# Kernel optimization log

Hardware: AMD Instinct MI355X
Metric: run time of the kernel (lower is better)

Reference implementation:

```python
import jax, jax.numpy as jnp
import numpy as np
import math

B, A, IN_C, OUT_C = 64, 128, 128, 64

def _l2norm(x, eps=1e-12):
    # matches F.normalize(dim=1) on 2D input: x / max(||x||_2, eps) along last dim
    n = jnp.sqrt(jnp.sum(x * x, axis=-1, keepdims=True))
    return x / jnp.maximum(n, eps)

def setup_inputs() -> dict:
    key = jax.random.key(0)
    ks = jax.random.split(key, 7)
    s = 1.0 / math.sqrt(IN_C)
    return {
        "features": jax.random.normal(ks[0], (B, IN_C, A), dtype=jnp.float32),
        "Wq": jax.random.uniform(ks[1], (OUT_C, IN_C), jnp.float32, -s, s),
        "bq": jax.random.uniform(ks[2], (OUT_C,), jnp.float32, -s, s),
        "Wk": jax.random.uniform(ks[3], (OUT_C, IN_C), jnp.float32, -s, s),
        "bk": jax.random.uniform(ks[4], (OUT_C,), jnp.float32, -s, s),
        "Wv": jax.random.uniform(ks[5], (OUT_C, IN_C), jnp.float32, -s, s),
        "bv": jax.random.uniform(ks[6], (OUT_C,), jnp.float32, -s, s),
    }

def reference(features, Wq, bq, Wk, bk, Wv, bv):
    b = features.shape[0]
    f = jnp.transpose(features, (0, 2, 1))          # (b, a, in_c)
    a = f.shape[1]
    q = f @ Wq.T + bq                               # (b, a, d)
    k = f @ Wk.T + bk
    v = f @ Wv.T + bv
    d = q.shape[-1]
    qf = q.reshape(-1, d)                           # (N, d), N = b*a
    kf = k.reshape(-1, d)
    vf = v.reshape(-1, d)
    att = jax.nn.softmax(qf @ kf.T / math.sqrt(d), axis=1)  # (N, N)
    qkv = att @ vf                                  # (N, d)
    qkv_n = _l2norm(qkv).reshape(b, a, d)
    v_n = _l2norm(vf).reshape(b, a, d)
    # sim_s[i,j] = (1/a) * sum_t v_n[i,t] . qkv_n[j,t]  (diagonal-trace over 'a')
    sim_s = jnp.einsum('bad,cad->bc', v_n, qkv_n) / a
    return sim_s
```

## Files before the change

### kernel.cpp

```cpp
#include <hip/hip_runtime.h>
#include <hip/hip_bf16.h>

#define NROW 8192
#define INC  128
#define OUTC 64

#define QSCALE 0.18033688011112042f

typedef __bf16 bf16x8 __attribute__((ext_vector_type(8)));
typedef __bf16 bf16x4 __attribute__((ext_vector_type(4)));
typedef short  s16x4  __attribute__((ext_vector_type(4)));
typedef float  f32x4  __attribute__((ext_vector_type(4)));

static __device__ __forceinline__ f32x4 mfma16(bf16x8 a, bf16x8 b, f32x4 c) {
    return __builtin_amdgcn_mfma_f32_16x16x32_bf16(a, b, c, 0, 0, 0);
}
static __device__ __forceinline__ f32x4 mfma1k(s16x4 a, s16x4 b, f32x4 c) {
    return __builtin_amdgcn_mfma_f32_16x16x16bf16_1k(a, b, c, 0, 0, 0);
}

static __device__ __forceinline__ bf16x8 cvt8(float4 lo, float4 hi) {
    bf16x8 r;
    r[0] = (__bf16)lo.x; r[1] = (__bf16)lo.y; r[2] = (__bf16)lo.z; r[3] = (__bf16)lo.w;
    r[4] = (__bf16)hi.x; r[5] = (__bf16)hi.y; r[6] = (__bf16)hi.z; r[7] = (__bf16)hi.w;
    return r;
}

__global__ __launch_bounds__(256) void proj_kernel(
    const float* __restrict__ feat,
    const float* __restrict__ Wq, const float* __restrict__ bq,
    const float* __restrict__ Wk, const float* __restrict__ bk,
    const float* __restrict__ Wv, const float* __restrict__ bv,
    __hip_bfloat16* __restrict__ qbf, __hip_bfloat16* __restrict__ kbf,
    __hip_bfloat16* __restrict__ vbf, __hip_bfloat16* __restrict__ vnb)
{
    __shared__ float slab[32 * 132];
    __shared__ float vbuf[32 * 66];
    __shared__ float invb[32];

    const int blk = blockIdx.x;
    const int mat = blk >> 8;
    const int b   = (blk >> 2) & 63;
    const int a0  = (blk & 3) * 32;
    const int r0  = b * 128 + a0;
    const float* fb = feat + (size_t)b * INC * 128;

    for (int i = threadIdx.x; i < 32 * 128; i += 256) {
        int c = i >> 5, a = i & 31;
        slab[a * 132 + c] = fb[c * 128 + a0 + a];
    }
    __syncthreads();

    const int w    = threadIdx.x >> 6;
    const int lane = threadIdx.x & 63;
    const int l16  = lane & 15;
    const int quad = lane >> 4;
    const int n0   = w * 16;

    const float* W    = (mat == 0) ? Wq : (mat == 1) ? Wk : Wv;
    const float* bias = (mat == 0) ? bq : (mat == 1) ? bk : bv;

    f32x4 acc[2] = {{0.f,0.f,0.f,0.f},{0.f,0.f,0.f,0.f}};
    #pragma unroll
    for (int kc = 0; kc < 4; ++kc) {
        const int k0 = kc * 32 + quad * 8;
        const float* wr = W + (n0 + l16) * INC + k0;
        bf16x8 bfr = cvt8(*(const float4*)wr, *(const float4*)(wr + 4));
        #pragma unroll
        for (int u = 0; u < 2; ++u) {
            const float* ar = slab + (u * 16 + l16) * 132 + k0;
            bf16x8 afr = cvt8(*(const float4*)ar, *(const float4*)(ar + 4));
            acc[u] = mfma16(afr, bfr, acc[u]);
        }
    }
    const float bl = bias[n0 + l16];
    const float sc = (mat == 0) ? QSCALE : 1.0f;

    if (mat < 2) {
        __hip_bfloat16* dst = mat ? kbf : qbf;
        #pragma unroll
        for (int u = 0; u < 2; ++u) {
            const int base = ((((r0 >> 4) + u) * 4 + w) << 8) + l16;
            #pragma unroll
            for (int r = 0; r < 4; ++r)
                dst[base + (quad * 4 + r) * 16] = __float2bfloat16((acc[u][r] + bl) * sc);
        }
    } else {
        #pragma unroll
        for (int u = 0; u < 2; ++u)
            #pragma unroll
            for (int r = 0; r < 4; ++r)
                vbuf[(u * 16 + quad * 4 + r) * 66 + n0 + l16] = acc[u][r] + bl;
        __syncthreads();
        const int rl = threadIdx.x >> 3;
        const int jj = threadIdx.x & 7;
        float ss = 0.f;
        #pragma unroll
        for (int i = 0; i < 8; ++i) {
            float x = vbuf[rl * 66 + jj * 8 + i];
            ss += x * x;
        }
        ss += __shfl_xor(ss, 1, 64);
        ss += __shfl_xor(ss, 2, 64);
        ss += __shfl_xor(ss, 4, 64);
        if (jj == 0) invb[rl] = rsqrtf(fmaxf(ss, 1e-24f));
        __syncthreads();
        float inv = invb[rl];
        bf16x8 vp;
        #pragma unroll
        for (int i = 0; i < 8; ++i)
            vp[i] = (__bf16)(vbuf[rl * 66 + jj * 8 + i] * inv);
        *(bf16x8*)(vnb + (size_t)(r0 + rl) * 64 + jj * 8) = vp;
        const int tl = threadIdx.x & 15;
        const int n  = (threadIdx.x >> 4) & 3;
        const int s_ = threadIdx.x >> 6;
        bf16x8 pack;
        #pragma unroll
        for (int j = 0; j < 8; ++j) {
            int key = s_ * 8 + j;
            pack[j] = (__bf16)(vbuf[key * 66 + n * 16 + tl] * invb[key]);
        }
        const int base = ((((r0 >> 4) + (s_ >> 1)) * 4 + n) << 8) + tl * 16 + (s_ & 1) * 8;
        *(bf16x8*)(vbf + base) = pack;
    }
}

__global__ __launch_bounds__(256) void attn_kernel(
    const __hip_bfloat16* __restrict__ qbf,
    const __hip_bfloat16* __restrict__ kbf,
    const __hip_bfloat16* __restrict__ vbf,
    float* __restrict__ Opart, float* __restrict__ lpart)
{
    const int qb    = blockIdx.x >> 3;
    const int bg    = blockIdx.x & 7;
    const int w     = threadIdx.x >> 6;
    const int lane  = threadIdx.x & 63;
    const int l16   = lane & 15;
    const int quad  = lane >> 4;
    const int r0    = qb * 128 + w * 32;
    const int fo    = l16 * 16 + quad * 4;
    const int fo32  = l16 * 16 + (quad & 1) * 8;
    const int qh    = quad >> 1;

    bf16x8 qf32[2][2];
    #pragma unroll
    for (int u = 0; u < 2; ++u)
        #pragma unroll
        for (int p = 0; p < 2; ++p)
            qf32[u][p] = *(const bf16x8*)(qbf +
                ((((r0 >> 4) + u) * 4 + p * 2 + qh) << 8) + fo32);

    f32x4 of[2][4];
    float lp[2] = {0.f, 0.f};
    #pragma unroll
    for (int u = 0; u < 2; ++u)
        #pragma unroll
        for (int n = 0; n < 4; ++n)
            of[u][n] = (f32x4){0.f, 0.f, 0.f, 0.f};

    const int ck0 = bg * 64;
    const char* kpA = (const char*)kbf + ck0 * 2048 + qh * 512 + fo32 * 2;
    const char* kpB = kpA + 4096;
    const char* vpA = (const char*)vbf + ck0 * 2048 + fo * 2;
    const char* vpB = vpA + 4096;

    #pragma unroll 1
    for (int it = 0; it < 16; ++it) {
        bf16x8 kf[4][2];
        #pragma unroll
        for (int t = 0; t < 2; ++t)
            #pragma unroll
            for (int p = 0; p < 2; ++p) {
                kf[t][p]     = *(const bf16x8*)(kpA + t * 2048 + p * 1024);
                kf[t + 2][p] = *(const bf16x8*)(kpB + t * 2048 + p * 1024);
            }
        s16x4 vf[4][4];
        #pragma unroll
        for (int n = 0; n < 4; ++n)
            #pragma unroll
            for (int t = 0; t < 2; ++t) {
                vf[n][t]     = *(const s16x4*)(vpA + t * 2048 + n * 512);
                vf[n][t + 2] = *(const s16x4*)(vpB + t * 2048 + n * 512);
            }
        kpA += 8192; kpB += 8192; vpA += 8192; vpB += 8192;

        const f32x4 zero = (f32x4){0.f, 0.f, 0.f, 0.f};
        #pragma unroll
        for (int u = 0; u < 2; ++u) {
            f32x4 s[4];
            #pragma unroll
            for (int t = 0; t < 4; ++t) {
                s[t] = mfma16(kf[t][0], qf32[u][0], zero);
                s[t] = mfma16(kf[t][1], qf32[u][1], s[t]);
            }
            #pragma unroll
            for (int t = 0; t < 4; ++t) {
                union { bf16x4 v; s16x4 s4; } pf;
                #pragma unroll
                for (int r = 0; r < 4; ++r) {
                    float p = __builtin_amdgcn_exp2f(s[t][r]);
                    lp[u] += p;
                    pf.v[r] = (__bf16)p;
                }
                #pragma unroll
                for (int n = 0; n < 4; ++n)
                    of[u][n] = mfma1k(pf.s4, vf[n][t], of[u][n]);
            }
        }
    }

    #pragma unroll
    for (int u = 0; u < 2; ++u) {
        float v = lp[u];
        v += __shfl_xor(v, 16, 64);
        v += __shfl_xor(v, 32, 64);
        lp[u] = v;
    }

    const int task = (qb * 4 + w) * 8 + bg;
    float* Ob = Opart + (size_t)task * 2048;
    #pragma unroll
    for (int u = 0; u < 2; ++u)
        #pragma unroll
        for (int n = 0; n < 4; ++n)
            #pragma unroll
            for (int r = 0; r < 4; ++r)
                Ob[(u * 16 + quad * 4 + r) * 64 + n * 16 + l16] = of[u][n][r];
    if (quad == 0) {
        lpart[task * 32 + l16]      = lp[0];
        lpart[task * 32 + 16 + l16] = lp[1];
    }
}

__global__ __launch_bounds__(256) void combine_kernel(
    const float* __restrict__ Opart, const float* __restrict__ lpart,
    __hip_bfloat16* __restrict__ qnb)
{
    const int r    = blockIdx.x * 4 + (threadIdx.x >> 6);
    const int c    = threadIdx.x & 63;
    const int tile = r >> 5, row = r & 31;
    float acc = 0.f, lsum = 0.f;
    #pragma unroll
    for (int g = 0; g < 8; ++g) {
        int task = tile * 8 + g;
        acc  += Opart[(size_t)task * 2048 + row * 64 + c];
        lsum += lpart[task * 32 + row];
    }
    float q = acc / lsum;
    float ss = q * q;
    ss += __shfl_xor(ss, 1, 64);
    ss += __shfl_xor(ss, 2, 64);
    ss += __shfl_xor(ss, 4, 64);
    ss += __shfl_xor(ss, 8, 64);
    ss += __shfl_xor(ss, 16, 64);
    ss += __shfl_xor(ss, 32, 64);
    qnb[(size_t)r * 64 + c] = __float2bfloat16(q * rsqrtf(fmaxf(ss, 1e-24f)));
}

__global__ __launch_bounds__(64) void sim_kernel(
    const __hip_bfloat16* __restrict__ vnb,
    const __hip_bfloat16* __restrict__ qnb,
    float* __restrict__ out)
{
    const int lane = threadIdx.x;
    const int l16  = lane & 15;
    const int quad = lane >> 4;
    const int kblk = blockIdx.x * 256;

    f32x4 acc[4][4];
    #pragma unroll
    for (int mi = 0; mi < 4; ++mi)
        #pragma unroll
        for (int ni = 0; ni < 4; ++ni)
            acc[mi][ni] = (f32x4){0.f, 0.f, 0.f, 0.f};

    #pragma unroll
    for (int ks = 0; ks < 8; ++ks) {
        const int k0 = kblk + ks * 32 + quad * 8;
        bf16x8 af[4], bfv[4];
        #pragma unroll
        for (int mi = 0; mi < 4; ++mi)
            af[mi] = *(const bf16x8*)(vnb + (size_t)(mi * 16 + l16) * 8192 + k0);
        #pragma unroll
        for (int ni = 0; ni < 4; ++ni)
            bfv[ni] = *(const bf16x8*)(qnb + (size_t)(ni * 16 + l16) * 8192 + k0);
        #pragma unroll
        for (int mi = 0; mi < 4; ++mi)
            #pragma unroll
            for (int ni = 0; ni < 4; ++ni)
                acc[mi][ni] = mfma16(af[mi], bfv[ni], acc[mi][ni]);
    }

    #pragma unroll
    for (int mi = 0; mi < 4; ++mi)
        #pragma unroll
        for (int ni = 0; ni < 4; ++ni)
            #pragma unroll
            for (int r = 0; r < 4; ++r)
                atomicAdd(&out[(mi * 16 + quad * 4 + r) * 64 + ni * 16 + l16],
                          acc[mi][ni][r] * (1.f / 128.f));
}

extern "C" void kernel_launch(void* const* d_in, const int* in_sizes, int n_in,
                              void* d_out, int out_size, void* d_ws, size_t ws_size,
                              hipStream_t stream)
{
    const float* feat = (const float*)d_in[0];
    const float* Wq   = (const float*)d_in[1];
    const float* bq   = (const float*)d_in[2];
    const float* Wk   = (const float*)d_in[3];
    const float* bk   = (const float*)d_in[4];
    const float* Wv   = (const float*)d_in[5];
    const float* bv   = (const float*)d_in[6];
    float* out = (float*)d_out;

    const size_t MB = 1u << 20;
    char* ws = (char*)d_ws;
    __hip_bfloat16* qbf = (__hip_bfloat16*)(ws);
    __hip_bfloat16* kbf = (__hip_bfloat16*)(ws + 1 * MB);
    __hip_bfloat16* vbf = (__hip_bfloat16*)(ws + 2 * MB);
    __hip_bfloat16* vnb = (__hip_bfloat16*)(ws + 3 * MB);
    float* Opart = (float*)(ws + 4 * MB);
    float* lpart = (float*)(ws + 20 * MB);
    __hip_bfloat16* qnb = (__hip_bfloat16*)(ws + 21 * MB);

    (void)hipMemsetAsync(out, 0, 64 * 64 * sizeof(float), stream);
    proj_kernel<<<768, 256, 0, stream>>>(feat, Wq, bq, Wk, bk, Wv, bv, qbf, kbf, vbf, vnb);
    attn_kernel<<<512, 256, 0, stream>>>(qbf, kbf, vbf, Opart, lpart);
    combine_kernel<<<2048, 256, 0, stream>>>(Opart, lpart, qnb);
    sim_kernel<<<32, 64, 0, stream>>>(vnb, qnb, out);
}
```

Measured before the change: 121.9 us.

## Give each attention wave 64 query rows and split keys 16 ways with repacked V

Each wave now handles 64 query rows instead of 32, so every loaded K/V fragment feeds twice as many MFMAs. Blocks shrink to two waves and the key range is split into 16 groups instead of 8. V is repacked in the projection kernel so each lane fetches it with wide 16-byte loads instead of 8-byte loads. The cost is more accumulator registers per wave, which may lower occupancy, and twice as much partial output (32 MB) for the combine kernel to read back, which moves the later workspace offsets.

New measurement: 124.6 us. 2.2% more time.

```diff
diff --git a/kernel.cpp b/kernel.cpp
--- a/kernel.cpp
+++ b/kernel.cpp
@@ -114,58 +114,62 @@
         const int tl = threadIdx.x & 15;
         const int n  = (threadIdx.x >> 4) & 3;
         const int s_ = threadIdx.x >> 6;
-        bf16x8 pack;
-        #pragma unroll
-        for (int j = 0; j < 8; ++j) {
-            int key = s_ * 8 + j;
-            pack[j] = (__bf16)(vbuf[key * 66 + n * 16 + tl] * invb[key]);
-        }
-        const int base = ((((r0 >> 4) + (s_ >> 1)) * 4 + n) << 8) + tl * 16 + (s_ & 1) * 8;
-        *(bf16x8*)(vbf + base) = pack;
-    }
-}
-
-__global__ __launch_bounds__(256) void attn_kernel(
+        const int h  = s_ >> 1;
+        const int p  = r0 >> 5;
+        __hip_bfloat16* vb = vbf + (size_t)(p * 4 + n) * 512 + tl * 32 + h * 4;
+        bf16x4 w0, w1;
+        #pragma unroll
+        for (int j = 0; j < 4; ++j) {
+            int k0 = s_ * 8 + j;
+            int k1 = s_ * 8 + 4 + j;
+            w0[j] = (__bf16)(vbuf[k0 * 66 + n * 16 + tl] * invb[k0]);
+            w1[j] = (__bf16)(vbuf[k1 * 66 + n * 16 + tl] * invb[k1]);
+        }
+        *(bf16x4*)(vb + ((s_ * 2) & 3) * 8)     = w0;
+        *(bf16x4*)(vb + ((s_ * 2 + 1) & 3) * 8) = w1;
+    }
+}
+
+__global__ __launch_bounds__(128) void attn_kernel(
     const __hip_bfloat16* __restrict__ qbf,
     const __hip_bfloat16* __restrict__ kbf,
     const __hip_bfloat16* __restrict__ vbf,
     float* __restrict__ Opart, float* __restrict__ lpart)
 {
-    const int qb    = blockIdx.x >> 3;
-    const int bg    = blockIdx.x & 7;
+    const int qb    = blockIdx.x >> 4;
+    const int bg    = blockIdx.x & 15;
     const int w     = threadIdx.x >> 6;
     const int lane  = threadIdx.x & 63;
     const int l16   = lane & 15;
     const int quad  = lane >> 4;
-    const int r0    = qb * 128 + w * 32;
-    const int fo    = l16 * 16 + quad * 4;
+    const int r0    = qb * 128 + w * 64;
     const int fo32  = l16 * 16 + (quad & 1) * 8;
     const int qh    = quad >> 1;
 
-    bf16x8 qf32[2][2];
-    #pragma unroll
-    for (int u = 0; u < 2; ++u)
+    bf16x8 qf32[4][2];
+    #pragma unroll
+    for (int u = 0; u < 4; ++u)
         #pragma unroll
         for (int p = 0; p < 2; ++p)
             qf32[u][p] = *(const bf16x8*)(qbf +
                 ((((r0 >> 4) + u) * 4 + p * 2 + qh) << 8) + fo32);
 
-    f32x4 of[2][4];
-    float lp[2] = {0.f, 0.f};
-    #pragma unroll
-    for (int u = 0; u < 2; ++u)
+    f32x4 of[4][4];
+    float lp[4] = {0.f, 0.f, 0.f, 0.f};
+    #pragma unroll
+    for (int u = 0; u < 4; ++u)
         #pragma unroll
         for (int n = 0; n < 4; ++n)
             of[u][n] = (f32x4){0.f, 0.f, 0.f, 0.f};
 
-    const int ck0 = bg * 64;
+    const int ck0 = bg * 32;
     const char* kpA = (const char*)kbf + ck0 * 2048 + qh * 512 + fo32 * 2;
     const char* kpB = kpA + 4096;
-    const char* vpA = (const char*)vbf + ck0 * 2048 + fo * 2;
+    const char* vpA = (const char*)vbf + (bg * 16) * 4096 + l16 * 64 + quad * 16;
     const char* vpB = vpA + 4096;
 
     #pragma unroll 1
-    for (int it = 0; it < 16; ++it) {
+    for (int it = 0; it < 8; ++it) {
         bf16x8 kf[4][2];
         #pragma unroll
         for (int t = 0; t < 2; ++t)
@@ -174,19 +178,17 @@
                 kf[t][p]     = *(const bf16x8*)(kpA + t * 2048 + p * 1024);
                 kf[t + 2][p] = *(const bf16x8*)(kpB + t * 2048 + p * 1024);
             }
-        s16x4 vf[4][4];
-        #pragma unroll
-        for (int n = 0; n < 4; ++n)
-            #pragma unroll
-            for (int t = 0; t < 2; ++t) {
-                vf[n][t]     = *(const s16x4*)(vpA + t * 2048 + n * 512);
-                vf[n][t + 2] = *(const s16x4*)(vpB + t * 2048 + n * 512);
-            }
+        bf16x8 vq[4][2];
+        #pragma unroll
+        for (int n = 0; n < 4; ++n) {
+            vq[n][0] = *(const bf16x8*)(vpA + n * 1024);
+            vq[n][1] = *(const bf16x8*)(vpB + n * 1024);
+        }
         kpA += 8192; kpB += 8192; vpA += 8192; vpB += 8192;
 
         const f32x4 zero = (f32x4){0.f, 0.f, 0.f, 0.f};
         #pragma unroll
-        for (int u = 0; u < 2; ++u) {
+        for (int u = 0; u < 4; ++u) {
             f32x4 s[4];
             #pragma unroll
             for (int t = 0; t < 4; ++t) {
@@ -203,32 +205,35 @@
                     pf.v[r] = (__bf16)p;
                 }
                 #pragma unroll
-                for (int n = 0; n < 4; ++n)
-                    of[u][n] = mfma1k(pf.s4, vf[n][t], of[u][n]);
+                for (int n = 0; n < 4; ++n) {
+                    s16x4 vh = ((const s16x4*)&vq[n][t >> 1])[t & 1];
+                    of[u][n] = mfma1k(pf.s4, vh, of[u][n]);
+                }
             }
         }
     }
 
     #pragma unroll
-    for (int u = 0; u < 2; ++u) {
+    for (int u = 0; u < 4; ++u) {
         float v = lp[u];
         v += __shfl_xor(v, 16, 64);
         v += __shfl_xor(v, 32, 64);
         lp[u] = v;
     }
 
-    const int task = (qb * 4 + w) * 8 + bg;
-    float* Ob = Opart + (size_t)task * 2048;
-    #pragma unroll
-    for (int u = 0; u < 2; ++u)
+    const int task = (qb * 2 + w) * 16 + bg;
+    float* Ob = Opart + (size_t)task * 4096;
+    #pragma unroll
+    for (int u = 0; u < 4; ++u)
         #pragma unroll
         for (int n = 0; n < 4; ++n)
             #pragma unroll
             for (int r = 0; r < 4; ++r)
                 Ob[(u * 16 + quad * 4 + r) * 64 + n * 16 + l16] = of[u][n][r];
     if (quad == 0) {
-        lpart[task * 32 + l16]      = lp[0];
-        lpart[task * 32 + 16 + l16] = lp[1];
+        #pragma unroll
+        for (int u = 0; u < 4; ++u)
+            lpart[task * 64 + u * 16 + l16] = lp[u];
     }
 }
 
@@ -236,15 +241,15 @@
     const float* __restrict__ Opart, const float* __restrict__ lpart,
     __hip_bfloat16* __restrict__ qnb)
 {
-    const int r    = blockIdx.x * 4 + (threadIdx.x >> 6);
-    const int c    = threadIdx.x & 63;
-    const int tile = r >> 5, row = r & 31;
+    const int r   = blockIdx.x * 4 + (threadIdx.x >> 6);
+    const int c   = threadIdx.x & 63;
+    const int t64 = r >> 6, row = r & 63;
     float acc = 0.f, lsum = 0.f;
     #pragma unroll
-    for (int g = 0; g < 8; ++g) {
-        int task = tile * 8 + g;
-        acc  += Opart[(size_t)task * 2048 + row * 64 + c];
-        lsum += lpart[task * 32 + row];
+    for (int g = 0; g < 16; ++g) {
+        int task = t64 * 16 + g;
+        acc  += Opart[(size_t)task * 4096 + row * 64 + c];
+        lsum += lpart[task * 64 + row];
     }
     float q = acc / lsum;
     float ss = q * q;
@@ -321,12 +326,12 @@
     __hip_bfloat16* vbf = (__hip_bfloat16*)(ws + 2 * MB);
     __hip_bfloat16* vnb = (__hip_bfloat16*)(ws + 3 * MB);
     float* Opart = (float*)(ws + 4 * MB);
-    float* lpart = (float*)(ws + 20 * MB);
-    __hip_bfloat16* qnb = (__hip_bfloat16*)(ws + 21 * MB);
+    float* lpart = (float*)(ws + 36 * MB);
+    __hip_bfloat16* qnb = (__hip_bfloat16*)(ws + 37 * MB);
 
     (void)hipMemsetAsync(out, 0, 64 * 64 * sizeof(float), stream);
     proj_kernel<<<768, 256, 0, stream>>>(feat, Wq, bq, Wk, bk, Wv, bv, qbf, kbf, vbf, vnb);
-    attn_kernel<<<512, 256, 0, stream>>>(qbf, kbf, vbf, Opart, lpart);
+    attn_kernel<<<1024, 128, 0, stream>>>(qbf, kbf, vbf, Opart, lpart);
     combine_kernel<<<2048, 256, 0, stream>>>(Opart, lpart, qnb);
     sim_kernel<<<32, 64, 0, stream>>>(vnb, qnb, out);
 }
```
